# Performance work log

Measured on AMD Instinct MI355X. Metric: run time of the kernel, lower is better.

Reference implementation:

```python
import jax, jax.numpy as jnp
import numpy as np

N_NODES = 50000
N_EDGES = 800000
IN_DIM, HID_DIM, OUT_DIM = 128, 64, 64


def spmm(row, col, val, dense):
    # sparse [N,N] (COO) @ dense [N,D] -> [N,D]
    gathered = dense[col] * val[:, None]          # [E, D]
    return jax.ops.segment_sum(gathered, row, num_segments=N_NODES)


def setup_inputs() -> dict:
    key = jax.random.key(0)
    ks = jax.random.split(key, 8)
    stdv1 = 1.0 / np.sqrt(HID_DIM)
    stdv2 = 1.0 / np.sqrt(OUT_DIM)
    return {
        "x": jax.random.normal(ks[0], (N_NODES, IN_DIM), dtype=jnp.float32),
        "edge_row": jax.random.randint(ks[1], (N_EDGES,), 0, N_NODES, dtype=jnp.int32),
        "edge_col": jax.random.randint(ks[2], (N_EDGES,), 0, N_NODES, dtype=jnp.int32),
        "edge_val": jax.random.uniform(ks[3], (N_EDGES,), dtype=jnp.float32),
        "W1": jax.random.uniform(ks[4], (IN_DIM, HID_DIM), jnp.float32, -stdv1, stdv1),
        "b1": jax.random.uniform(ks[5], (HID_DIM,), jnp.float32, -stdv1, stdv1),
        "W2": jax.random.uniform(ks[6], (HID_DIM, OUT_DIM), jnp.float32, -stdv2, stdv2),
        "b2": jax.random.uniform(ks[7], (OUT_DIM,), jnp.float32, -stdv2, stdv2),
    }


def reference(x, edge_row, edge_col, edge_val, W1, b1, W2, b2):
    # layer 1: support = x @ W1; out = adj @ support + b1; relu
    h = jax.nn.relu(spmm(edge_row, edge_col, edge_val, x @ W1) + b1)
    # dropout: eval mode (training=False) -> identity
    # layer 2
    return spmm(edge_row, edge_col, edge_val, h @ W2) + b2
```

## Files before the change

### kernel.cpp

```cpp
#include <hip/hip_runtime.h>


#define N_NODES 50000
#define N_EDGES 800000
#define IN_DIM  128
#define HID_DIM 64
#define OUT_DIM 64

#define NB   196
#define EPB  4096
#define NBLK_E ((N_EDGES + EPB - 1) / EPB)
#define BCAP 5120

typedef __attribute__((ext_vector_type(8))) short bf16x8;
typedef __attribute__((ext_vector_type(4))) float f32x4;

__device__ inline unsigned short f2bf(float x) {
    unsigned u = __float_as_uint(x);
    return (unsigned short)((u + 0x7FFFu + ((u >> 16) & 1u)) >> 16);
}
__device__ inline float bf2f(unsigned v) {
    return __uint_as_float(v << 16);
}

__global__ __launch_bounds__(256) void k_prep(
    const float* __restrict__ W1, unsigned short* __restrict__ Wt1,
    const float* __restrict__ W2, unsigned short* __restrict__ Wt2,
    int* __restrict__ bcur)
{
    int b = blockIdx.x, t = threadIdx.x;
    if (b < 32) {
        int e = b * 256 + t;
        int c = e / IN_DIM, k = e % IN_DIM;
        Wt1[c * IN_DIM + k] = f2bf(W1[k * HID_DIM + c]);
    } else if (b < 48) {
        int e2 = (b - 32) * 256 + t;
        int c = e2 / HID_DIM, k = e2 % HID_DIM;
        Wt2[c * HID_DIM + k] = f2bf(W2[k * OUT_DIM + c]);
    } else {
        if (t < NB) bcur[t] = 0;
    }
}

__global__ __launch_bounds__(256) void k_bscatter(
    const int* __restrict__ erow, const int* __restrict__ ecol,
    const float* __restrict__ eval_, int* __restrict__ bcur,
    uint2* __restrict__ bucketed)
{
    __shared__ int lc[NB];
    __shared__ int lbase[NB];
    int t = threadIdx.x;
    for (int i = t; i < NB; i += 256) lc[i] = 0;
    __syncthreads();
    int base = blockIdx.x * EPB;
    int bkt[16], rnk[16];
    #pragma unroll 4
    for (int i = 0; i < 16; ++i) {
        int e = base + i * 256 + t;
        bkt[i] = -1;
        if (e < N_EDGES) {
            bkt[i] = erow[e] >> 8;
            rnk[i] = atomicAdd(&lc[bkt[i]], 1);
        }
    }
    __syncthreads();
    for (int i = t; i < NB; i += 256)
        lbase[i] = lc[i] ? atomicAdd(&bcur[i], lc[i]) : 0;
    __syncthreads();
    #pragma unroll 4
    for (int i = 0; i < 16; ++i) {
        int e = base + i * 256 + t;
        if (bkt[i] >= 0) {
            unsigned r = (unsigned)erow[e];
            unsigned w0 = (unsigned)ecol[e] | ((r & 255u) << 16);
            bucketed[(size_t)bkt[i] * BCAP + lbase[bkt[i]] + rnk[i]] =
                make_uint2(w0, __float_as_uint(eval_[e]));
        }
    }
}

__global__ __launch_bounds__(256) void k_bfinal(
    const int* __restrict__ bcur, const uint2* __restrict__ bucketed,
    uint2* __restrict__ pairs, int2* __restrict__ offs2)
{
    __shared__ uint2 ebuf[BCAP];
    __shared__ int rcnt[256];
    __shared__ int rsc[256];
    int t = threadIdx.x, b = blockIdx.x;
    int ne = bcur[b];
    int base0 = b * BCAP;
    rcnt[t] = 0;
    __syncthreads();
    for (int i = t; i < ne; i += 256) {
        uint2 p = bucketed[(size_t)base0 + i];
        ebuf[i] = p;
        atomicAdd(&rcnt[(p.x >> 16) & 255], 1);
    }
    __syncthreads();
    int v = rcnt[t];
    rsc[t] = v;
    __syncthreads();
    #pragma unroll
    for (int off = 1; off < 256; off <<= 1) {
        int add = (t >= off) ? rsc[t - off] : 0;
        __syncthreads();
        rsc[t] += add;
        __syncthreads();
    }
    int start = base0 + rsc[t] - v;
    int gr = (b << 8) + t;
    if (gr < N_NODES) offs2[gr] = make_int2(start, start + v);
    rcnt[t] = start;
    __syncthreads();
    for (int i = t; i < ne; i += 256) {
        uint2 p = ebuf[i];
        int pos = atomicAdd(&rcnt[(p.x >> 16) & 255], 1);
        pairs[pos] = make_uint2(p.x & 0xFFFFu, p.y);
    }
}

template <bool APPLY_RELU, bool OUT_BF16>
__global__ __launch_bounds__(256) void k_gather(
    const int2* __restrict__ offs2, const uint2* __restrict__ pairs,
    const unsigned short* __restrict__ dense, const float* __restrict__ bias,
    void* __restrict__ outp)
{
    int t = threadIdx.x;
    int r = __builtin_amdgcn_readfirstlane(blockIdx.x * 4 + (t >> 6));
    int d = t & 63;
    int2 oe = offs2[r];
    int e0 = oe.x, e1 = oe.y;
    float a[8];
    a[0] = bias[d];
    #pragma unroll
    for (int i = 1; i < 8; ++i) a[i] = 0.f;
    int e = e0;
    for (; e + 8 <= e1; e += 8) {
        uint2 p[8];
        #pragma unroll
        for (int i = 0; i < 8; ++i) p[i] = pairs[e + i];
        unsigned v[8];
        #pragma unroll
        for (int i = 0; i < 8; ++i) v[i] = dense[(size_t)p[i].x * 64u + d];
        #pragma unroll
        for (int i = 0; i < 8; ++i)
            a[i] = fmaf(__uint_as_float(p[i].y), bf2f(v[i]), a[i]);
    }
    if (e + 4 <= e1) {
        uint2 p[4];
        #pragma unroll
        for (int i = 0; i < 4; ++i) p[i] = pairs[e + i];
        unsigned v[4];
        #pragma unroll
        for (int i = 0; i < 4; ++i) v[i] = dense[(size_t)p[i].x * 64u + d];
        #pragma unroll
        for (int i = 0; i < 4; ++i)
            a[i] = fmaf(__uint_as_float(p[i].y), bf2f(v[i]), a[i]);
        e += 4;
    }
    for (; e < e1; ++e) {
        uint2 p = pairs[e];
        a[0] = fmaf(__uint_as_float(p.y),
                    bf2f(dense[(size_t)p.x * 64u + d]), a[0]);
    }
    float acc = ((a[0] + a[1]) + (a[2] + a[3])) +
                ((a[4] + a[5]) + (a[6] + a[7]));
    if (APPLY_RELU) acc = fmaxf(acc, 0.f);
    if (OUT_BF16)
        ((unsigned short*)outp)[(size_t)r * 64 + d] = f2bf(acc);
    else
        ((float*)outp)[(size_t)r * 64 + d] = acc;
}

template <int K, bool IN_BF16>
__global__ __launch_bounds__(256) void k_gemm_mfma(
    const void* __restrict__ Xv, const unsigned short* __restrict__ Wt,
    unsigned short* __restrict__ out)
{
    __shared__ unsigned short Al[32 * K];
    __shared__ unsigned short Bl[64 * K];
    int t = threadIdx.x;
    int m0 = blockIdx.x * 32;

    #pragma unroll
    for (int i = 0; i < K / 32; ++i) {
        int u4 = i * 256 + t;
        int col = (u4 * 8) / K, k = (u4 * 8) % K;
        uint4 w = ((const uint4*)Wt)[u4];
        int byte = (col * K + k) * 2;
        byte ^= ((col & 7) << 4);
        *(uint4*)((char*)Bl + byte) = w;
    }
    if (IN_BF16) {
        const unsigned short* X = (const unsigned short*)Xv;
        int row = t / (K / 8), k = (t % (K / 8)) * 8;
        int grow = m0 + row;
        uint4 v = make_uint4(0, 0, 0, 0);
        if (grow < N_NODES)
            v = *(const uint4*)(X + (size_t)grow * K + k);
        int byte = (row * K + k) * 2;
        byte ^= ((row & 7) << 4);
        *(uint4*)((char*)Al + byte) = v;
    } else {
        const float* X = (const float*)Xv;
        #pragma unroll
        for (int i = 0; i < K / 64; ++i) {
            int f8 = i * 256 + t;
            int row = (f8 * 8) / K, k = (f8 * 8) % K;
            int grow = m0 + row;
            float4 xa = make_float4(0.f, 0.f, 0.f, 0.f), xb = xa;
            if (grow < N_NODES) {
                const float4* src = (const float4*)(X + (size_t)grow * K + k);
                xa = src[0];
                xb = src[1];
            }
            uint4 v;
            v.x = (unsigned)f2bf(xa.x) | ((unsigned)f2bf(xa.y) << 16);
            v.y = (unsigned)f2bf(xa.z) | ((unsigned)f2bf(xa.w) << 16);
            v.z = (unsigned)f2bf(xb.x) | ((unsigned)f2bf(xb.y) << 16);
            v.w = (unsigned)f2bf(xb.z) | ((unsigned)f2bf(xb.w) << 16);
            int byte = (row * K + k) * 2;
            byte ^= ((row & 7) << 4);
            *(uint4*)((char*)Al + byte) = v;
        }
    }
    __syncthreads();

    int w = t >> 6, l = t & 63;
    int lr0 = (w & 1) * 16;
    int c0  = (w >> 1) * 32;
    int lrow = lr0 + (l & 15);
    int kb = (l >> 4) * 8;
    int col0 = c0 + (l & 15), col1 = col0 + 16;
    f32x4 acc0 = {0.f, 0.f, 0.f, 0.f}, acc1 = {0.f, 0.f, 0.f, 0.f};
    #pragma unroll
    for (int kc = 0; kc < K / 32; ++kc) {
        int ka = kc * 32 + kb;
        int ab = (lrow * K + ka) * 2;  ab ^= ((lrow & 7) << 4);
        int bb0 = (col0 * K + ka) * 2; bb0 ^= ((col0 & 7) << 4);
        int bb1 = (col1 * K + ka) * 2; bb1 ^= ((col1 & 7) << 4);
        bf16x8 a  = *(const bf16x8*)((const char*)Al + ab);
        bf16x8 b0 = *(const bf16x8*)((const char*)Bl + bb0);
        bf16x8 b1 = *(const bf16x8*)((const char*)Bl + bb1);
        acc0 = __builtin_amdgcn_mfma_f32_16x16x32_bf16(a, b0, acc0, 0, 0, 0);
        acc1 = __builtin_amdgcn_mfma_f32_16x16x32_bf16(a, b1, acc1, 0, 0, 0);
    }
    int grow0 = m0 + lr0 + (l >> 4) * 4;
    #pragma unroll
    for (int j = 0; j < 4; ++j) {
        int gr = grow0 + j;
        if (gr < N_NODES) {
            out[(size_t)gr * 64 + col0] = f2bf(acc0[j]);
            out[(size_t)gr * 64 + col1] = f2bf(acc1[j]);
        }
    }
}

extern "C" void kernel_launch(void* const* d_in, const int* in_sizes, int n_in,
                              void* d_out, int out_size, void* d_ws, size_t ws_size,
                              hipStream_t stream)
{
    const float* x     = (const float*)d_in[0];
    const int*   erow  = (const int*)d_in[1];
    const int*   ecol  = (const int*)d_in[2];
    const float* eval_ = (const float*)d_in[3];
    const float* W1    = (const float*)d_in[4];
    const float* b1    = (const float*)d_in[5];
    const float* W2    = (const float*)d_in[6];
    const float* b2    = (const float*)d_in[7];
    float* out = (float*)d_out;

    uint2* pairs    = (uint2*)d_ws;
    uint2* bucketed = pairs + (size_t)NB * BCAP;
    unsigned short* support = (unsigned short*)(bucketed + (size_t)NB * BCAP);
    unsigned short* agg1 = support + (size_t)N_NODES * 64;
    unsigned short* Wt1 = agg1 + (size_t)N_NODES * 64;
    unsigned short* Wt2 = Wt1 + IN_DIM * HID_DIM;
    int*  bcur  = (int*)(Wt2 + HID_DIM * OUT_DIM);
    int2* offs2 = (int2*)(bcur + NB + 2);

    const int row_grid  = N_NODES / 4;
    const int gemm_grid = (N_NODES + 31) / 32;

    k_prep<<<49, 256, 0, stream>>>(W1, Wt1, W2, Wt2, bcur);
    k_bscatter<<<NBLK_E, 256, 0, stream>>>(erow, ecol, eval_, bcur, bucketed);
    k_bfinal<<<NB, 256, 0, stream>>>(bcur, bucketed, pairs, offs2);

    k_gemm_mfma<IN_DIM, false><<<gemm_grid, 256, 0, stream>>>(x, Wt1, support);
    k_gather<true, true><<<row_grid, 256, 0, stream>>>(offs2, pairs, support, b1, agg1);
    k_gemm_mfma<HID_DIM, true><<<gemm_grid, 256, 0, stream>>>(agg1, Wt2, support);
    k_gather<false, false><<<row_grid, 256, 0, stream>>>(offs2, pairs, support, b2, out);
}
```

Before: 95.07 us.

## Fuse first GEMM and edge bucket-scatter into one heterogeneous kernel launch

```diff
diff --git a/kernel.cpp b/kernel.cpp
--- a/kernel.cpp
+++ b/kernel.cpp
@@ -11,6 +11,7 @@
 #define EPB  4096
 #define NBLK_E ((N_EDGES + EPB - 1) / EPB)
 #define BCAP 5120
+#define GEMM1_GRID ((N_NODES + 31) / 32)
 
 typedef __attribute__((ext_vector_type(8))) short bf16x8;
 typedef __attribute__((ext_vector_type(4))) float f32x4;
@@ -42,146 +43,13 @@
     }
 }
 
-__global__ __launch_bounds__(256) void k_bscatter(
-    const int* __restrict__ erow, const int* __restrict__ ecol,
-    const float* __restrict__ eval_, int* __restrict__ bcur,
-    uint2* __restrict__ bucketed)
-{
-    __shared__ int lc[NB];
-    __shared__ int lbase[NB];
-    int t = threadIdx.x;
-    for (int i = t; i < NB; i += 256) lc[i] = 0;
-    __syncthreads();
-    int base = blockIdx.x * EPB;
-    int bkt[16], rnk[16];
-    #pragma unroll 4
-    for (int i = 0; i < 16; ++i) {
-        int e = base + i * 256 + t;
-        bkt[i] = -1;
-        if (e < N_EDGES) {
-            bkt[i] = erow[e] >> 8;
-            rnk[i] = atomicAdd(&lc[bkt[i]], 1);
-        }
-    }
-    __syncthreads();
-    for (int i = t; i < NB; i += 256)
-        lbase[i] = lc[i] ? atomicAdd(&bcur[i], lc[i]) : 0;
-    __syncthreads();
-    #pragma unroll 4
-    for (int i = 0; i < 16; ++i) {
-        int e = base + i * 256 + t;
-        if (bkt[i] >= 0) {
-            unsigned r = (unsigned)erow[e];
-            unsigned w0 = (unsigned)ecol[e] | ((r & 255u) << 16);
-            bucketed[(size_t)bkt[i] * BCAP + lbase[bkt[i]] + rnk[i]] =
-                make_uint2(w0, __float_as_uint(eval_[e]));
-        }
-    }
-}
-
-__global__ __launch_bounds__(256) void k_bfinal(
-    const int* __restrict__ bcur, const uint2* __restrict__ bucketed,
-    uint2* __restrict__ pairs, int2* __restrict__ offs2)
-{
-    __shared__ uint2 ebuf[BCAP];
-    __shared__ int rcnt[256];
-    __shared__ int rsc[256];
-    int t = threadIdx.x, b = blockIdx.x;
-    int ne = bcur[b];
-    int base0 = b * BCAP;
-    rcnt[t] = 0;
-    __syncthreads();
-    for (int i = t; i < ne; i += 256) {
-        uint2 p = bucketed[(size_t)base0 + i];
-        ebuf[i] = p;
-        atomicAdd(&rcnt[(p.x >> 16) & 255], 1);
-    }
-    __syncthreads();
-    int v = rcnt[t];
-    rsc[t] = v;
-    __syncthreads();
-    #pragma unroll
-    for (int off = 1; off < 256; off <<= 1) {
-        int add = (t >= off) ? rsc[t - off] : 0;
-        __syncthreads();
-        rsc[t] += add;
-        __syncthreads();
-    }
-    int start = base0 + rsc[t] - v;
-    int gr = (b << 8) + t;
-    if (gr < N_NODES) offs2[gr] = make_int2(start, start + v);
-    rcnt[t] = start;
-    __syncthreads();
-    for (int i = t; i < ne; i += 256) {
-        uint2 p = ebuf[i];
-        int pos = atomicAdd(&rcnt[(p.x >> 16) & 255], 1);
-        pairs[pos] = make_uint2(p.x & 0xFFFFu, p.y);
-    }
-}
-
-template <bool APPLY_RELU, bool OUT_BF16>
-__global__ __launch_bounds__(256) void k_gather(
-    const int2* __restrict__ offs2, const uint2* __restrict__ pairs,
-    const unsigned short* __restrict__ dense, const float* __restrict__ bias,
-    void* __restrict__ outp)
-{
-    int t = threadIdx.x;
-    int r = __builtin_amdgcn_readfirstlane(blockIdx.x * 4 + (t >> 6));
-    int d = t & 63;
-    int2 oe = offs2[r];
-    int e0 = oe.x, e1 = oe.y;
-    float a[8];
-    a[0] = bias[d];
-    #pragma unroll
-    for (int i = 1; i < 8; ++i) a[i] = 0.f;
-    int e = e0;
-    for (; e + 8 <= e1; e += 8) {
-        uint2 p[8];
-        #pragma unroll
-        for (int i = 0; i < 8; ++i) p[i] = pairs[e + i];
-        unsigned v[8];
-        #pragma unroll
-        for (int i = 0; i < 8; ++i) v[i] = dense[(size_t)p[i].x * 64u + d];
-        #pragma unroll
-        for (int i = 0; i < 8; ++i)
-            a[i] = fmaf(__uint_as_float(p[i].y), bf2f(v[i]), a[i]);
-    }
-    if (e + 4 <= e1) {
-        uint2 p[4];
-        #pragma unroll
-        for (int i = 0; i < 4; ++i) p[i] = pairs[e + i];
-        unsigned v[4];
-        #pragma unroll
-        for (int i = 0; i < 4; ++i) v[i] = dense[(size_t)p[i].x * 64u + d];
-        #pragma unroll
-        for (int i = 0; i < 4; ++i)
-            a[i] = fmaf(__uint_as_float(p[i].y), bf2f(v[i]), a[i]);
-        e += 4;
-    }
-    for (; e < e1; ++e) {
-        uint2 p = pairs[e];
-        a[0] = fmaf(__uint_as_float(p.y),
-                    bf2f(dense[(size_t)p.x * 64u + d]), a[0]);
-    }
-    float acc = ((a[0] + a[1]) + (a[2] + a[3])) +
-                ((a[4] + a[5]) + (a[6] + a[7]));
-    if (APPLY_RELU) acc = fmaxf(acc, 0.f);
-    if (OUT_BF16)
-        ((unsigned short*)outp)[(size_t)r * 64 + d] = f2bf(acc);
-    else
-        ((float*)outp)[(size_t)r * 64 + d] = acc;
-}
-
 template <int K, bool IN_BF16>
-__global__ __launch_bounds__(256) void k_gemm_mfma(
+__device__ __forceinline__ void gemm_body(
+    unsigned short* __restrict__ Al, unsigned short* __restrict__ Bl,
     const void* __restrict__ Xv, const unsigned short* __restrict__ Wt,
-    unsigned short* __restrict__ out)
-{
-    __shared__ unsigned short Al[32 * K];
-    __shared__ unsigned short Bl[64 * K];
-    int t = threadIdx.x;
-    int m0 = blockIdx.x * 32;
-
+    unsigned short* __restrict__ out, int bid, int t)
+{
+    int m0 = bid * 32;
     #pragma unroll
     for (int i = 0; i < K / 32; ++i) {
         int u4 = i * 256 + t;
@@ -256,6 +124,155 @@
     }
 }
 
+__global__ __launch_bounds__(256) void k_mega1(
+    const float* __restrict__ X, const unsigned short* __restrict__ Wt1,
+    unsigned short* __restrict__ support,
+    const int* __restrict__ erow, const int* __restrict__ ecol,
+    const float* __restrict__ eval_, int* __restrict__ bcur,
+    uint2* __restrict__ bucketed)
+{
+    __shared__ __align__(16) unsigned char smem[24576];
+    int t = threadIdx.x;
+    if (blockIdx.x < GEMM1_GRID) {
+        gemm_body<IN_DIM, false>((unsigned short*)smem,
+                                 (unsigned short*)(smem + 8192),
+                                 X, Wt1, support, blockIdx.x, t);
+        return;
+    }
+    int* lc    = (int*)smem;
+    int* lbase = lc + NB;
+    int blk = blockIdx.x - GEMM1_GRID;
+    for (int i = t; i < NB; i += 256) lc[i] = 0;
+    __syncthreads();
+    int base = blk * EPB;
+    int bkt[16], rnk[16];
+    #pragma unroll 4
+    for (int i = 0; i < 16; ++i) {
+        int e = base + i * 256 + t;
+        bkt[i] = -1;
+        if (e < N_EDGES) {
+            bkt[i] = erow[e] >> 8;
+            rnk[i] = atomicAdd(&lc[bkt[i]], 1);
+        }
+    }
+    __syncthreads();
+    for (int i = t; i < NB; i += 256)
+        lbase[i] = lc[i] ? atomicAdd(&bcur[i], lc[i]) : 0;
+    __syncthreads();
+    #pragma unroll 4
+    for (int i = 0; i < 16; ++i) {
+        int e = base + i * 256 + t;
+        if (bkt[i] >= 0) {
+            unsigned r = (unsigned)erow[e];
+            unsigned w0 = (unsigned)ecol[e] | ((r & 255u) << 16);
+            bucketed[(size_t)bkt[i] * BCAP + lbase[bkt[i]] + rnk[i]] =
+                make_uint2(w0, __float_as_uint(eval_[e]));
+        }
+    }
+}
+
+__global__ __launch_bounds__(256) void k_bfinal(
+    const int* __restrict__ bcur, const uint2* __restrict__ bucketed,
+    uint2* __restrict__ pairs, int2* __restrict__ offs2)
+{
+    __shared__ uint2 ebuf[BCAP];
+    __shared__ int rcnt[256];
+    __shared__ int rsc[256];
+    int t = threadIdx.x, b = blockIdx.x;
+    int ne = bcur[b];
+    int base0 = b * BCAP;
+    rcnt[t] = 0;
+    __syncthreads();
+    for (int i = t; i < ne; i += 256) {
+        uint2 p = bucketed[(size_t)base0 + i];
+        ebuf[i] = p;
+        atomicAdd(&rcnt[(p.x >> 16) & 255], 1);
+    }
+    __syncthreads();
+    int v = rcnt[t];
+    rsc[t] = v;
+    __syncthreads();
+    #pragma unroll
+    for (int off = 1; off < 256; off <<= 1) {
+        int add = (t >= off) ? rsc[t - off] : 0;
+        __syncthreads();
+        rsc[t] += add;
+        __syncthreads();
+    }
+    int start = base0 + rsc[t] - v;
+    int gr = (b << 8) + t;
+    if (gr < N_NODES) offs2[gr] = make_int2(start, start + v);
+    rcnt[t] = start;
+    __syncthreads();
+    for (int i = t; i < ne; i += 256) {
+        uint2 p = ebuf[i];
+        int pos = atomicAdd(&rcnt[(p.x >> 16) & 255], 1);
+        pairs[pos] = make_uint2(p.x & 0xFFFFu, p.y);
+    }
+}
+
+template <bool APPLY_RELU, bool OUT_BF16>
+__global__ __launch_bounds__(256) void k_gather(
+    const int2* __restrict__ offs2, const uint2* __restrict__ pairs,
+    const unsigned short* __restrict__ dense, const float* __restrict__ bias,
+    void* __restrict__ outp)
+{
+    int t = threadIdx.x;
+    int r = __builtin_amdgcn_readfirstlane(blockIdx.x * 4 + (t >> 6));
+    int d = t & 63;
+    int2 oe = offs2[r];
+    int e0 = oe.x, e1 = oe.y;
+    float a[8];
+    a[0] = bias[d];
+    #pragma unroll
+    for (int i = 1; i < 8; ++i) a[i] = 0.f;
+    int e = e0;
+    for (; e + 8 <= e1; e += 8) {
+        uint2 p[8];
+        #pragma unroll
+        for (int i = 0; i < 8; ++i) p[i] = pairs[e + i];
+        unsigned v[8];
+        #pragma unroll
+        for (int i = 0; i < 8; ++i) v[i] = dense[(size_t)p[i].x * 64u + d];
+        #pragma unroll
+        for (int i = 0; i < 8; ++i)
+            a[i] = fmaf(__uint_as_float(p[i].y), bf2f(v[i]), a[i]);
+    }
+    if (e + 4 <= e1) {
+        uint2 p[4];
+        #pragma unroll
+        for (int i = 0; i < 4; ++i) p[i] = pairs[e + i];
+        unsigned v[4];
+        #pragma unroll
+        for (int i = 0; i < 4; ++i) v[i] = dense[(size_t)p[i].x * 64u + d];
+        #pragma unroll
+        for (int i = 0; i < 4; ++i)
+            a[i] = fmaf(__uint_as_float(p[i].y), bf2f(v[i]), a[i]);
+        e += 4;
+    }
+    for (; e < e1; ++e) {
+        uint2 p = pairs[e];
+        a[0] = fmaf(__uint_as_float(p.y),
+                    bf2f(dense[(size_t)p.x * 64u + d]), a[0]);
+    }
+    float acc = ((a[0] + a[1]) + (a[2] + a[3])) +
+                ((a[4] + a[5]) + (a[6] + a[7]));
+    if (APPLY_RELU) acc = fmaxf(acc, 0.f);
+    if (OUT_BF16)
+        ((unsigned short*)outp)[(size_t)r * 64 + d] = f2bf(acc);
+    else
+        ((float*)outp)[(size_t)r * 64 + d] = acc;
+}
+
+__global__ __launch_bounds__(256) void k_gemm2(
+    const unsigned short* __restrict__ X, const unsigned short* __restrict__ Wt,
+    unsigned short* __restrict__ out)
+{
+    __shared__ unsigned short Al[32 * HID_DIM];
+    __shared__ unsigned short Bl[64 * HID_DIM];
+    gemm_body<HID_DIM, true>(Al, Bl, X, Wt, out, blockIdx.x, threadIdx.x);
+}
+
 extern "C" void kernel_launch(void* const* d_in, const int* in_sizes, int n_in,
                               void* d_out, int out_size, void* d_ws, size_t ws_size,
                               hipStream_t stream)
@@ -279,15 +296,15 @@
     int*  bcur  = (int*)(Wt2 + HID_DIM * OUT_DIM);
     int2* offs2 = (int2*)(bcur + NB + 2);
 
-    const int row_grid  = N_NODES / 4;
-    const int gemm_grid = (N_NODES + 31) / 32;
+    const int row_grid = N_NODES / 4;
 
     k_prep<<<49, 256, 0, stream>>>(W1, Wt1, W2, Wt2, bcur);
-    k_bscatter<<<NBLK_E, 256, 0, stream>>>(erow, ecol, eval_, bcur, bucketed);
+    k_mega1<<<GEMM1_GRID + NBLK_E, 256, 0, stream>>>(
+        x, Wt1, support, erow, ecol, eval_, bcur, bucketed);
     k_bfinal<<<NB, 256, 0, stream>>>(bcur, bucketed, pairs, offs2);
-
-    k_gemm_mfma<IN_DIM, false><<<gemm_grid, 256, 0, stream>>>(x, Wt1, support);
-    k_gather<true, true><<<row_grid, 256, 0, stream>>>(offs2, pairs, support, b1, agg1);
-    k_gemm_mfma<HID_DIM, true><<<gemm_grid, 256, 0, stream>>>(agg1, Wt2, support);
-    k_gather<false, false><<<row_grid, 256, 0, stream>>>(offs2, pairs, support, b2, out);
-}
+    k_gather<true, true><<<row_grid, 256, 0, stream>>>(
+        offs2, pairs, support, b1, agg1);
+    k_gemm2<<<GEMM1_GRID, 256, 0, stream>>>(agg1, Wt2, support);
+    k_gather<false, false><<<row_grid, 256, 0, stream>>>(
+        offs2, pairs, support, b2, out);
+}
```

New measurement: 94.95 us. About the same (-0.1%).
